# Optimization experiments

Measured on AMD Instinct MI355X. Metric: run time of the kernel, lower is better.

The kernel has to match this reference:

```python
import jax, jax.numpy as jnp
import numpy as np

HID, BOT, C, HEADS, K, SCALES, HZN = 32, 8, 16, 4, 3, 4, 12


def layer_norm(x, g, b, eps=1e-5):
    m = jnp.mean(x, axis=-1, keepdims=True)
    v = jnp.var(x, axis=-1, keepdims=True)
    return (x - m) * jax.lax.rsqrt(v + eps) * g + b


def setup_inputs() -> dict:
    B, T, N = 8, 32, 1500
    keys = iter(jax.random.split(jax.random.key(0), 64))
    def nrm(shape, s=0.05):
        return jax.random.normal(next(keys), shape, jnp.float32) * s
    x = jax.random.normal(next(keys), (B, T, N), jnp.float32)
    adj = (jax.random.uniform(next(keys), (N, N)) < 0.01).astype(jnp.float32)
    return dict(
        x=x, adj=adj,
        dw_w=nrm((1, 1, K)), dw_b=jnp.zeros((1,)),
        bn1_g=jnp.ones((1,)), bn1_b=jnp.zeros((1,)),
        pw_w=nrm((C, 1)), pw_b=jnp.zeros((C,)),
        bn2_g=jnp.ones((C,)), bn2_b=jnp.zeros((C,)),
        feat_w=nrm((C, HID)), feat_b=jnp.zeros((HID,)),
        scale_w=nrm((SCALES, HID, HID)), scale_b=jnp.zeros((SCALES, HID)),
        scale_ln_g=jnp.ones((SCALES, HID)), scale_ln_b=jnp.zeros((SCALES, HID)),
        fusion_weight=jnp.exp(-0.5 * jnp.arange(SCALES, dtype=jnp.float32)),
        fus_lo_w=nrm((HID, BOT)), fus_lo_b=jnp.zeros((BOT,)),
        fus_hi_w=nrm((BOT, HID)), fus_hi_b=jnp.zeros((HID,)),
        sp_ln_g=jnp.ones((HID,)), sp_ln_b=jnp.zeros((HID,)),
        qkv_lo_w=nrm((HID, 3 * BOT)), qkv_lo_b=jnp.zeros((3 * BOT,)),
        qkv_hi_w=nrm((3 * BOT, 3 * HID)), qkv_hi_b=jnp.zeros((3 * HID,)),
        graph_U=nrm((N, BOT)), graph_V=nrm((BOT, N)),
        adj_mix=jnp.array(0.0, jnp.float32), adj_scale=jnp.array(1.0, jnp.float32),
        out_lo_w=nrm((HID, BOT)), out_lo_b=jnp.zeros((BOT,)),
        out_hi_w=nrm((BOT, HID)), out_hi_b=jnp.zeros((HID,)),
        at_ln_g=jnp.ones((HID,)), at_ln_b=jnp.zeros((HID,)),
        pred_lo_w=nrm((HID, BOT)), pred_lo_b=jnp.zeros((BOT,)),
        mid_ln_g=jnp.ones((BOT,)), mid_ln_b=jnp.zeros((BOT,)),
        pred_hi_w=nrm((BOT, HZN)), pred_hi_b=jnp.zeros((HZN,)),
        log_decay=jnp.array(-2.3, jnp.float32),
        gate_w1=nrm((HID, BOT)), gate_b1=jnp.zeros((BOT,)),
        gate_w2=nrm((BOT, HZN)), gate_b2=jnp.zeros((HZN,)),
    )


def reference(x, adj, dw_w, dw_b, bn1_g, bn1_b, pw_w, pw_b, bn2_g, bn2_b,
              feat_w, feat_b, scale_w, scale_b, scale_ln_g, scale_ln_b,
              fusion_weight, fus_lo_w, fus_lo_b, fus_hi_w, fus_hi_b,
              sp_ln_g, sp_ln_b, qkv_lo_w, qkv_lo_b, qkv_hi_w, qkv_hi_b,
              graph_U, graph_V, adj_mix, adj_scale,
              out_lo_w, out_lo_b, out_hi_w, out_hi_b, at_ln_g, at_ln_b,
              pred_lo_w, pred_lo_b, mid_ln_g, mid_ln_b, pred_hi_w, pred_hi_b,
              log_decay, gate_w1, gate_b1, gate_w2, gate_b2):
    B, T, N = x.shape
    # ---- temporal feature extraction: depthwise-separable conv, eval-mode BN ----
    s = x.transpose(0, 2, 1).reshape(B * N, 1, T)  # per-node series [B*N,1,T]
    dw = jax.lax.conv_general_dilated(
        s, dw_w, (1,), 'SAME', dimension_numbers=('NCH', 'OIH', 'NCH'))
    dw = jax.nn.relu((dw + dw_b[None, :, None]) * bn1_g[None, :, None] + bn1_b[None, :, None])
    pw = jnp.einsum('bit,oi->bot', dw, pw_w) + pw_b[None, :, None]  # pointwise 1x1
    pw = jax.nn.relu(pw * bn2_g[None, :, None] + bn2_b[None, :, None])
    h = pw.mean(-1).reshape(B, N, C) @ feat_w + feat_b  # [B,N,HID]
    # ---- multi-scale spatial diffusion over adjacency powers ----
    eye = jnp.eye(N, dtype=x.dtype)
    a_hat = adj + eye
    a_hat = a_hat / (jnp.sum(a_hat, axis=-1, keepdims=True) + 1e-8)
    a2 = a_hat @ a_hat
    hops = [eye, a_hat, a2, a2 @ a_hat]
    feats = []
    for i in range(SCALES):  # fixed, small loop over scales
        agg = h if i == 0 else jnp.einsum('nm,bmh->bnh', hops[i], h)
        t = agg @ scale_w[i] + scale_b[i]
        feats.append(jax.nn.relu(layer_norm(t, scale_ln_g[i], scale_ln_b[i])))
    alpha = jax.nn.softmax(fusion_weight)
    fused = sum(alpha[i] * feats[i] for i in range(SCALES))
    out = (fused @ fus_lo_w + fus_lo_b) @ fus_hi_w + fus_hi_b  # bottleneck fusion
    h = layer_norm(out + h, sp_ln_g, sp_ln_b)
    # ---- low-rank adaptive graph attention ----
    qkv = (h @ qkv_lo_w + qkv_lo_b) @ qkv_hi_w + qkv_hi_b  # [B,N,3*HID]
    q, k, v = jnp.split(qkv, 3, axis=-1)
    hd = HID // HEADS
    to_heads = lambda t: t.reshape(B, N, HEADS, hd).transpose(0, 2, 1, 3)
    q, k, v = to_heads(q), to_heads(k), to_heads(v)
    scores = jnp.einsum('bhnd,bhmd->bhnm', q, k) / jnp.sqrt(jnp.float32(hd))
    struct = graph_U @ graph_V + jax.nn.sigmoid(adj_mix) * adj_scale * adj  # [N,N]
    attn = jax.nn.softmax(scores + struct[None, None], axis=-1)
    o = jnp.einsum('bhnm,bhmd->bhnd', attn, v).transpose(0, 2, 1, 3).reshape(B, N, HID)
    o = (o @ out_lo_w + out_lo_b) @ out_hi_w + out_hi_b
    h = layer_norm(o + h, at_ln_g, at_ln_b)
    # ---- gated horizon predictor with learned exponential decay ----
    x_mid = jax.nn.relu(layer_norm(h @ pred_lo_w + pred_lo_b, mid_ln_g, mid_ln_b))
    init_pred = x_mid @ pred_hi_w + pred_hi_b  # [B,N,HZN]
    gate = jax.nn.sigmoid(jax.nn.relu(h @ gate_w1 + gate_b1) @ gate_w2 + gate_b2)
    tdec = jnp.arange(1, HZN + 1, dtype=x.dtype)  # [HZN]
    prog = x[:, -1, :, None] * jnp.exp(-jnp.exp(log_decay) * tdec)
    return gate * init_pred + (1.0 - gate) * prog
```

## Files before the change

kernel.cpp:

```cpp
#include <hip/hip_runtime.h>
#include <math.h>

#define NN 1500
#define BB 8
#define TT 32
#define HIDD 32
#define BOTT 8
#define CC 16
#define NHEADS 4
#define NSCALES 4
#define HZNN 12
#define BC (BB*HIDD)
#define CAP 128
#define MC 128
#define MSPLIT 2
#define RT 128
#define NTILES 12
#define PROWS (NTILES*RT)

__global__ void k_prep_temporal(const float* __restrict__ adj,
                                const float* __restrict__ gV,
                                int* __restrict__ sidx, float* __restrict__ sval,
                                float* __restrict__ sraw, int* __restrict__ scnt,
                                float* __restrict__ VgT,
                                const float* __restrict__ x,
    const float* __restrict__ dw_w, const float* __restrict__ dw_b,
    const float* __restrict__ bn1_g, const float* __restrict__ bn1_b,
    const float* __restrict__ pw_w, const float* __restrict__ pw_b,
    const float* __restrict__ bn2_g, const float* __restrict__ bn2_b,
    const float* __restrict__ feat_w, const float* __restrict__ feat_b,
    float* __restrict__ h0) {
  if (blockIdx.x < NN) {
    int n = blockIdx.x;
    int tid = threadIdx.x;
    const float* row = adj + (size_t)n * NN;
    __shared__ int cnt;
    __shared__ float red[4];
    __shared__ float s_inv;
    float ssum = 0.f;
    for (int m = tid; m < NN; m += 256) ssum += row[m];
    for (int off = 32; off > 0; off >>= 1) ssum += __shfl_down(ssum, off, 64);
    if ((tid & 63) == 0) red[tid >> 6] = ssum;
    if (tid == 0) cnt = 0;
    __syncthreads();
    if (tid == 0) {
      float tot = red[0] + red[1] + red[2] + red[3] + 1.0f;
      s_inv = 1.0f / (tot + 1e-8f);
    }
    __syncthreads();
    float inv = s_inv;
    for (int m = tid; m < NN; m += 256) {
      float a = row[m];
      if (a != 0.f || m == n) {
        int pos = atomicAdd(&cnt, 1);
        if (pos < CAP) {
          sidx[n * CAP + pos] = m;
          sval[n * CAP + pos] = (a + (m == n ? 1.f : 0.f)) * inv;
          sraw[n * CAP + pos] = a;
        }
      }
    }
    __syncthreads();
    if (tid == 0) scnt[n] = min(cnt, CAP);
    if (n == 0) {
      for (int m = tid; m < NN; m += 256) {
#pragma unroll
        for (int j = 0; j < 8; ++j) VgT[m * 8 + j] = gV[j * NN + m];
      }
    }
  } else {
    int tid = (blockIdx.x - NN) * 256 + threadIdx.x;
    if (tid >= BB * NN) return;
    int b = tid / NN, n = tid % NN;
    float s[TT];
#pragma unroll
    for (int t = 0; t < TT; ++t) s[t] = x[(size_t)b * TT * NN + (size_t)t * NN + n];
    float w0 = dw_w[0], w1 = dw_w[1], w2 = dw_w[2];
    float db = dw_b[0], g1v = bn1_g[0], b1v = bn1_b[0];
    float dwr[TT];
#pragma unroll
    for (int t = 0; t < TT; ++t) {
      float left  = (t > 0)      ? s[t - 1] : 0.f;
      float right = (t < TT - 1) ? s[t + 1] : 0.f;
      float v = left * w0 + s[t] * w1 + right * w2;
      v = (v + db) * g1v + b1v;
      dwr[t] = fmaxf(v, 0.f);
    }
    float mo[CC];
#pragma unroll
    for (int o = 0; o < CC; ++o) mo[o] = 0.f;
    for (int t = 0; t < TT; ++t) {
      float d = dwr[t];
#pragma unroll
      for (int o = 0; o < CC; ++o) {
        float v = (d * pw_w[o] + pw_b[o]) * bn2_g[o] + bn2_b[o];
        mo[o] += fmaxf(v, 0.f);
      }
    }
#pragma unroll
    for (int o = 0; o < CC; ++o) mo[o] *= (1.f / TT);
    float* dst = h0 + (size_t)n * BC + b * HIDD;
    for (int j = 0; j < HIDD; ++j) {
      float acc = feat_b[j];
#pragma unroll
      for (int o = 0; o < CC; ++o) acc += mo[o] * feat_w[o * HIDD + j];
      dst[j] = acc;
    }
  }
}

__global__ void k_spmm_sp(const int* __restrict__ sidx, const float* __restrict__ sval,
                          const int* __restrict__ scnt,
                          const float* __restrict__ X, float* __restrict__ Y) {
  int n = blockIdx.x;
  int tid = threadIdx.x;
  __shared__ int   li[CAP];
  __shared__ float lv[CAP];
  int cnt = scnt[n];
  if (tid < cnt) { li[tid] = sidx[n * CAP + tid]; lv[tid] = sval[n * CAP + tid]; }
  __syncthreads();
  float acc = 0.f;
  for (int e = 0; e < cnt; ++e) acc += lv[e] * X[(size_t)li[e] * BC + tid];
  Y[(size_t)n * BC + tid] = acc;
}

__global__ void k_fuse_qkv(
    const float* __restrict__ h0, const float* __restrict__ g1,
    const float* __restrict__ g2, const float* __restrict__ g3,
    const float* __restrict__ scale_w, const float* __restrict__ scale_b,
    const float* __restrict__ sln_g, const float* __restrict__ sln_b,
    const float* __restrict__ fusion_w,
    const float* __restrict__ fus_lo_w, const float* __restrict__ fus_lo_b,
    const float* __restrict__ fus_hi_w, const float* __restrict__ fus_hi_b,
    const float* __restrict__ sp_g, const float* __restrict__ sp_b,
    const float* __restrict__ qkv_lo_w, const float* __restrict__ qkv_lo_b,
    const float* __restrict__ qkv_hi_w, const float* __restrict__ qkv_hi_b,
    float* __restrict__ h_out,
    float* __restrict__ Qw, float* __restrict__ Kw, float* __restrict__ Vw) {
  int tid = threadIdx.x;
  int gr = tid >> 4, l = tid & 15;
  int row = blockIdx.x * 16 + gr;
  int b = row / NN, n = row % NN;
  size_t rofs = (size_t)n * BC + b * HIDD;
  int j0 = 2 * l;
  float fw0 = fusion_w[0], fw1 = fusion_w[1], fw2 = fusion_w[2], fw3 = fusion_w[3];
  float fm = fmaxf(fmaxf(fw0, fw1), fmaxf(fw2, fw3));
  float e0 = __expf(fw0 - fm), e1 = __expf(fw1 - fm), e2 = __expf(fw2 - fm), e3 = __expf(fw3 - fm);
  float einv = 1.f / (e0 + e1 + e2 + e3);
  float alpha[4] = {e0 * einv, e1 * einv, e2 * einv, e3 * einv};
  const float* srcp[4] = {h0, g1, g2, g3};
  float fused[2] = {0.f, 0.f};
#pragma unroll
  for (int i = 0; i < NSCALES; ++i) {
    const float* sp = srcp[i] + rofs;
    float src[32];
#pragma unroll
    for (int k4 = 0; k4 < 8; ++k4) {
      float4 f = *(const float4*)(sp + k4 * 4);
      src[k4 * 4] = f.x; src[k4 * 4 + 1] = f.y; src[k4 * 4 + 2] = f.z; src[k4 * 4 + 3] = f.w;
    }
    const float* W = scale_w + i * HIDD * HIDD;
    float t0 = scale_b[i * HIDD + j0], t1v = scale_b[i * HIDD + j0 + 1];
#pragma unroll
    for (int k = 0; k < 32; ++k) {
      float2 w = *(const float2*)(W + k * HIDD + j0);
      t0 += src[k] * w.x; t1v += src[k] * w.y;
    }
    float s1 = t0 + t1v;
    float s2 = t0 * t0 + t1v * t1v;
    s1 += __shfl_xor(s1, 1, 16); s1 += __shfl_xor(s1, 2, 16);
    s1 += __shfl_xor(s1, 4, 16); s1 += __shfl_xor(s1, 8, 16);
    s2 += __shfl_xor(s2, 1, 16); s2 += __shfl_xor(s2, 2, 16);
    s2 += __shfl_xor(s2, 4, 16); s2 += __shfl_xor(s2, 8, 16);
    float mean = s1 * (1.f / 32.f);
    float var = s2 * (1.f / 32.f) - mean * mean;
    float r = rsqrtf(var + 1e-5f);
    float a = alpha[i];
    float tn0 = (t0 - mean) * r * sln_g[i * HIDD + j0] + sln_b[i * HIDD + j0];
    float tn1 = (t1v - mean) * r * sln_g[i * HIDD + j0 + 1] + sln_b[i * HIDD + j0 + 1];
    fused[0] += a * fmaxf(tn0, 0.f);
    fused[1] += a * fmaxf(tn1, 0.f);
  }
  float lo[BOTT];
#pragma unroll
  for (int o = 0; o < BOTT; ++o) {
    float acc = fused[0] * fus_lo_w[j0 * BOTT + o] + fused[1] * fus_lo_w[(j0 + 1) * BOTT + o];
    acc += __shfl_xor(acc, 1, 16); acc += __shfl_xor(acc, 2, 16);
    acc += __shfl_xor(acc, 4, 16); acc += __shfl_xor(acc, 8, 16);
    lo[o] = acc + fus_lo_b[o];
  }
  float2 hv2 = *(const float2*)(h0 + rofs + j0);
  float pre[2] = {hv2.x, hv2.y};
#pragma unroll
  for (int jj = 0; jj < 2; ++jj) {
    float acc = fus_hi_b[j0 + jj] + pre[jj];
#pragma unroll
    for (int o = 0; o < BOTT; ++o) acc += lo[o] * fus_hi_w[o * HIDD + j0 + jj];
    pre[jj] = acc;
  }
  {
    float s1 = pre[0] + pre[1];
    float s2 = pre[0] * pre[0] + pre[1] * pre[1];
    s1 += __shfl_xor(s1, 1, 16); s1 += __shfl_xor(s1, 2, 16);
    s1 += __shfl_xor(s1, 4, 16); s1 += __shfl_xor(s1, 8, 16);
    s2 += __shfl_xor(s2, 1, 16); s2 += __shfl_xor(s2, 2, 16);
    s2 += __shfl_xor(s2, 4, 16); s2 += __shfl_xor(s2, 8, 16);
    float mean = s1 * (1.f / 32.f);
    float var = s2 * (1.f / 32.f) - mean * mean;
    float r = rsqrtf(var + 1e-5f);
#pragma unroll
    for (int jj = 0; jj < 2; ++jj)
      pre[jj] = (pre[jj] - mean) * r * sp_g[j0 + jj] + sp_b[j0 + jj];
  }
  *(float2*)(h_out + (size_t)row * HIDD + j0) = make_float2(pre[0], pre[1]);
  float t1[24];
#pragma unroll
  for (int o = 0; o < 24; ++o) {
    float acc = pre[0] * qkv_lo_w[j0 * 24 + o] + pre[1] * qkv_lo_w[(j0 + 1) * 24 + o];
    acc += __shfl_xor(acc, 1, 16); acc += __shfl_xor(acc, 2, 16);
    acc += __shfl_xor(acc, 4, 16); acc += __shfl_xor(acc, 8, 16);
    t1[o] = acc + qkv_lo_b[o];
  }
  int sub = l >> 3, d = l & 7;
#pragma unroll
  for (int part = 0; part < 3; ++part) {
    float* dst = (part == 0) ? Qw : (part == 1) ? Kw : Vw;
#pragma unroll
    for (int hh = 0; hh < 2; ++hh) {
      int hd = sub * 2 + hh;
      int p = part * 32 + hd * 8 + d;
      float acc = qkv_hi_b[p];
#pragma unroll
      for (int o = 0; o < 24; ++o) acc += t1[o] * qkv_hi_w[o * 96 + p];
      dst[(((size_t)b * NHEADS + hd) * NN + n) * 8 + d] = acc;
    }
  }
}

__global__ void __launch_bounds__(256, 2)
k_attn(const float* __restrict__ Qw, const float* __restrict__ Kw,
       const float* __restrict__ Vw,
       const float* __restrict__ gU, const float* __restrict__ VgT,
       const int* __restrict__ sidx, const float* __restrict__ sraw,
       const int* __restrict__ scnt,
       const float* __restrict__ adj_mix, const float* __restrict__ adj_scale,
       float* __restrict__ P) {
  int bh = blockIdx.x, tile = blockIdx.y, z = blockIdx.z;
  int tid = threadIdx.x;
  int g = tid >> 3, p = tid & 7;
  __shared__ float Ks[MC * 20];
  __shared__ float Vs[MC * 12];
  const float scl = 0.35355339059327373f;
  float qv[4][16], acc[4][8], sm[4];
  int nrow[4];
#pragma unroll
  for (int rr = 0; rr < 4; ++rr) {
    int n = tile * RT + g * 4 + rr;
    nrow[rr] = n;
    int nc = (n < NN) ? n : NN - 1;
    const float* qp = Qw + ((size_t)bh * NN + nc) * 8;
    float4 q0 = *(const float4*)qp;
    float4 q1 = *(const float4*)(qp + 4);
    const float* up = gU + nc * 8;
    float4 u0 = *(const float4*)up;
    float4 u1 = *(const float4*)(up + 4);
    qv[rr][0] = q0.x * scl; qv[rr][1] = q0.y * scl; qv[rr][2] = q0.z * scl; qv[rr][3] = q0.w * scl;
    qv[rr][4] = q1.x * scl; qv[rr][5] = q1.y * scl; qv[rr][6] = q1.z * scl; qv[rr][7] = q1.w * scl;
    qv[rr][8] = u0.x; qv[rr][9] = u0.y; qv[rr][10] = u0.z; qv[rr][11] = u0.w;
    qv[rr][12] = u1.x; qv[rr][13] = u1.y; qv[rr][14] = u1.z; qv[rr][15] = u1.w;
    sm[rr] = 0.f;
#pragma unroll
    for (int d = 0; d < 8; ++d) acc[rr][d] = 0.f;
  }
  if (z < MSPLIT) {
    const int mcount = NN / MSPLIT;
    const int mbase = z * mcount;
    const float* Kb = Kw + (size_t)bh * NN * 8;
    const float* Vb = Vw + (size_t)bh * NN * 8;
    for (int c0 = 0; c0 < mcount; c0 += MC) {
      int mlen = min(MC, mcount - c0);
      __syncthreads();
      {
        int mm = tid >> 1, hh = tid & 1;
        float4 kf = make_float4(0.f,0.f,0.f,0.f), gf = kf, vf = kf;
        if (mm < mlen) {
          int m = mbase + c0 + mm;
          kf = *(const float4*)(Kb + (size_t)m * 8 + hh * 4);
          gf = *(const float4*)(VgT + (size_t)m * 8 + hh * 4);
          vf = *(const float4*)(Vb + (size_t)m * 8 + hh * 4);
        }
        *(float4*)(Ks + mm * 20 + hh * 4) = kf;
        *(float4*)(Ks + mm * 20 + 8 + hh * 4) = gf;
        *(float4*)(Vs + mm * 12 + hh * 4) = vf;
      }
      __syncthreads();
#pragma unroll 2
      for (int i = 0; i < MC / 8; ++i) {
        int mm = p + i * 8;
        const float* kp = Ks + mm * 20;
        float4 k0 = *(const float4*)(kp);
        float4 k1 = *(const float4*)(kp + 4);
        float4 k2 = *(const float4*)(kp + 8);
        float4 k3 = *(const float4*)(kp + 12);
        const float* vp = Vs + mm * 12;
        float4 v0 = *(const float4*)(vp);
        float4 v1 = *(const float4*)(vp + 4);
#pragma unroll
        for (int rr = 0; rr < 4; ++rr) {
          float s = qv[rr][0]*k0.x + qv[rr][1]*k0.y + qv[rr][2]*k0.z + qv[rr][3]*k0.w
                  + qv[rr][4]*k1.x + qv[rr][5]*k1.y + qv[rr][6]*k1.z + qv[rr][7]*k1.w
                  + qv[rr][8]*k2.x + qv[rr][9]*k2.y + qv[rr][10]*k2.z + qv[rr][11]*k2.w
                  + qv[rr][12]*k3.x + qv[rr][13]*k3.y + qv[rr][14]*k3.z + qv[rr][15]*k3.w;
          float e = __expf(s);
          sm[rr] += e;
          acc[rr][0] += e * v0.x; acc[rr][1] += e * v0.y; acc[rr][2] += e * v0.z; acc[rr][3] += e * v0.w;
          acc[rr][4] += e * v1.x; acc[rr][5] += e * v1.y; acc[rr][6] += e * v1.z; acc[rr][7] += e * v1.w;
        }
      }
      if (mlen < MC) {
        int npad = (MC / 8) - ((mlen - p + 7) >> 3);
#pragma unroll
        for (int rr = 0; rr < 4; ++rr) sm[rr] -= (float)npad;
      }
    }
  } else {
    float smix = adj_scale[0] / (1.f + __expf(-adj_mix[0]));
    const float* Kb = Kw + (size_t)bh * NN * 8;
    const float* Vb = Vw + (size_t)bh * NN * 8;
#pragma unroll
    for (int rr = 0; rr < 4; ++rr) {
      int n = nrow[rr];
      if (n < NN) {
        int cnt = scnt[n];
        for (int e = p; e < cnt; e += 8) {
          int m = sidx[n * CAP + e];
          float a = sraw[n * CAP + e];
          if (a != 0.f) {
            const float* kp = Kb + (size_t)m * 8;
            float4 k0 = *(const float4*)(kp);
            float4 k1 = *(const float4*)(kp + 4);
            const float* gp = VgT + (size_t)m * 8;
            float4 k2 = *(const float4*)(gp);
            float4 k3 = *(const float4*)(gp + 4);
            float s = qv[rr][0]*k0.x + qv[rr][1]*k0.y + qv[rr][2]*k0.z + qv[rr][3]*k0.w
                    + qv[rr][4]*k1.x + qv[rr][5]*k1.y + qv[rr][6]*k1.z + qv[rr][7]*k1.w
                    + qv[rr][8]*k2.x + qv[rr][9]*k2.y + qv[rr][10]*k2.z + qv[rr][11]*k2.w
                    + qv[rr][12]*k3.x + qv[rr][13]*k3.y + qv[rr][14]*k3.z + qv[rr][15]*k3.w;
            float ep = __expf(s);
            float dlt = ep * (__expf(smix * a) - 1.f);
            sm[rr] += dlt;
            const float* vp = Vb + (size_t)m * 8;
            float4 v0 = *(const float4*)(vp);
            float4 v1 = *(const float4*)(vp + 4);
            acc[rr][0] += dlt * v0.x; acc[rr][1] += dlt * v0.y; acc[rr][2] += dlt * v0.z; acc[rr][3] += dlt * v0.w;
            acc[rr][4] += dlt * v1.x; acc[rr][5] += dlt * v1.y; acc[rr][6] += dlt * v1.z; acc[rr][7] += dlt * v1.w;
          }
        }
      }
    }
  }
#pragma unroll
  for (int rr = 0; rr < 4; ++rr) {
    float s = sm[rr];
    s += __shfl_xor(s, 1, 8); s += __shfl_xor(s, 2, 8); s += __shfl_xor(s, 4, 8);
#pragma unroll
    for (int d = 0; d < 8; ++d) {
      acc[rr][d] += __shfl_xor(acc[rr][d], 1, 8);
      acc[rr][d] += __shfl_xor(acc[rr][d], 2, 8);
      acc[rr][d] += __shfl_xor(acc[rr][d], 4, 8);
    }
    float val = acc[rr][0];
#pragma unroll
    for (int d = 1; d < 8; ++d) if (p == d) val = acc[rr][d];
    if (nrow[rr] < NN) {
      float* dst = P + ((size_t)(z * 32 + bh) * PROWS + nrow[rr]) * 12;
      dst[p] = val;
      if (p == 0) dst[8] = s;
    }
  }
}

__global__ void k_final(const float* __restrict__ P, const float* __restrict__ h_in,
    const float* __restrict__ x,
    const float* __restrict__ out_lo_w, const float* __restrict__ out_lo_b,
    const float* __restrict__ out_hi_w, const float* __restrict__ out_hi_b,
    const float* __restrict__ at_g, const float* __restrict__ at_b,
    const float* __restrict__ pred_lo_w, const float* __restrict__ pred_lo_b,
    const float* __restrict__ mid_g, const float* __restrict__ mid_b,
    const float* __restrict__ pred_hi_w, const float* __restrict__ pred_hi_b,
    const float* __restrict__ log_decay,
    const float* __restrict__ gate_w1, const float* __restrict__ gate_b1,
    const float* __restrict__ gate_w2, const float* __restrict__ gate_b2,
    float* __restrict__ out) {
  int tid = threadIdx.x;
  int gr = tid >> 3, l = tid & 7;
  int row = blockIdx.x * 32 + gr;
  int b = row / NN, n = row % NN;
  int j0 = 4 * l;
  int hd = l >> 1, d0 = (l & 1) * 4;
  int bh = b * NHEADS + hd;
  float av[4] = {0.f, 0.f, 0.f, 0.f};
  float smt = 0.f;
#pragma unroll
  for (int z = 0; z <= MSPLIT; ++z) {
    const float* q = P + ((size_t)(z * 32 + bh) * PROWS + n) * 12;
    float4 a4 = *(const float4*)(q + d0);
    av[0] += a4.x; av[1] += a4.y; av[2] += a4.z; av[3] += a4.w;
    smt += q[8];
  }
  float oinv = 1.f / smt;
  float ov4[4];
#pragma unroll
  for (int d = 0; d < 4; ++d) ov4[d] = av[d] * oinv;
  float lo[BOTT];
#pragma unroll
  for (int o = 0; o < BOTT; ++o) {
    float acc = 0.f;
#pragma unroll
    for (int jj = 0; jj < 4; ++jj) acc += ov4[jj] * out_lo_w[(j0 + jj) * BOTT + o];
    acc += __shfl_xor(acc, 1, 8); acc += __shfl_xor(acc, 2, 8); acc += __shfl_xor(acc, 4, 8);
    lo[o] = acc + out_lo_b[o];
  }
  float4 hin4 = *(const float4*)(h_in + (size_t)row * HIDD + j0);
  float pre[4] = {hin4.x, hin4.y, hin4.z, hin4.w};
#pragma unroll
  for (int jj = 0; jj < 4; ++jj) {
    float acc = out_hi_b[j0 + jj] + pre[jj];
#pragma unroll
    for (int o = 0; o < BOTT; ++o) acc += lo[o] * out_hi_w[o * HIDD + j0 + jj];
    pre[jj] = acc;
  }
  float h2[4];
  {
    float s1 = pre[0] + pre[1] + pre[2] + pre[3];
    float s2 = pre[0]*pre[0] + pre[1]*pre[1] + pre[2]*pre[2] + pre[3]*pre[3];
    s1 += __shfl_xor(s1, 1, 8); s1 += __shfl_xor(s1, 2, 8); s1 += __shfl_xor(s1, 4, 8);
    s2 += __shfl_xor(s2, 1, 8); s2 += __shfl_xor(s2, 2, 8); s2 += __shfl_xor(s2, 4, 8);
    float mean = s1 * (1.f / 32.f);
    float var = s2 * (1.f / 32.f) - mean * mean;
    float r = rsqrtf(var + 1e-5f);
#pragma unroll
    for (int jj = 0; jj < 4; ++jj)
      h2[jj] = (pre[jj] - mean) * r * at_g[j0 + jj] + at_b[j0 + jj];
  }
  float pl[BOTT];
#pragma unroll
  for (int o = 0; o < BOTT; ++o) {
    float acc = 0.f;
#pragma unroll
    for (int jj = 0; jj < 4; ++jj) acc += h2[jj] * pred_lo_w[(j0 + jj) * BOTT + o];
    acc += __shfl_xor(acc, 1, 8); acc += __shfl_xor(acc, 2, 8); acc += __shfl_xor(acc, 4, 8);
    pl[o] = acc + pred_lo_b[o];
  }
  float xm[BOTT];
  {
    float m = 0.f;
#pragma unroll
    for (int o = 0; o < BOTT; ++o) m += pl[o];
    m *= (1.f / BOTT);
    float var = 0.f;
#pragma unroll
    for (int o = 0; o < BOTT; ++o) { float d = pl[o] - m; var += d * d; }
    var *= (1.f / BOTT);
    float r = rsqrtf(var + 1e-5f);
#pragma unroll
    for (int o = 0; o < BOTT; ++o)
      xm[o] = fmaxf((pl[o] - m) * r * mid_g[o] + mid_b[o], 0.f);
  }
  float ga[BOTT];
#pragma unroll
  for (int o = 0; o < BOTT; ++o) {
    float acc = 0.f;
#pragma unroll
    for (int jj = 0; jj < 4; ++jj) acc += h2[jj] * gate_w1[(j0 + jj) * BOTT + o];
    acc += __shfl_xor(acc, 1, 8); acc += __shfl_xor(acc, 2, 8); acc += __shfl_xor(acc, 4, 8);
    ga[o] = fmaxf(acc + gate_b1[o], 0.f);
  }
  float xl = x[(size_t)b * TT * NN + (size_t)(TT - 1) * NN + n];
  float dec = __expf(log_decay[0]);
#pragma unroll
  for (int ii = 0; ii < 2; ++ii) {
    int i = l + ii * 8;
    if (i < HZNN) {
      float accp = pred_hi_b[i];
#pragma unroll
      for (int o = 0; o < BOTT; ++o) accp += xm[o] * pred_hi_w[o * HZNN + i];
      float accg = gate_b2[i];
#pragma unroll
      for (int o = 0; o < BOTT; ++o) accg += ga[o] * gate_w2[o * HZNN + i];
      float gt = 1.f / (1.f + __expf(-accg));
      float pr = xl * __expf(-dec * (float)(i + 1));
      out[(size_t)row * HZNN + i] = gt * accp + (1.f - gt) * pr;
    }
  }
}

extern "C" void kernel_launch(void* const* d_in, const int* in_sizes, int n_in,
                              void* d_out, int out_size, void* d_ws, size_t ws_size,
                              hipStream_t stream) {
  const float* x          = (const float*)d_in[0];
  const float* adj        = (const float*)d_in[1];
  const float* dw_w       = (const float*)d_in[2];
  const float* dw_b       = (const float*)d_in[3];
  const float* bn1_g      = (const float*)d_in[4];
  const float* bn1_b      = (const float*)d_in[5];
  const float* pw_w       = (const float*)d_in[6];
  const float* pw_b       = (const float*)d_in[7];
  const float* bn2_g      = (const float*)d_in[8];
  const float* bn2_b      = (const float*)d_in[9];
  const float* feat_w     = (const float*)d_in[10];
  const float* feat_b     = (const float*)d_in[11];
  const float* scale_w    = (const float*)d_in[12];
  const float* scale_b    = (const float*)d_in[13];
  const float* scale_ln_g = (const float*)d_in[14];
  const float* scale_ln_b = (const float*)d_in[15];
  const float* fusion_w   = (const float*)d_in[16];
  const float* fus_lo_w   = (const float*)d_in[17];
  const float* fus_lo_b   = (const float*)d_in[18];
  const float* fus_hi_w   = (const float*)d_in[19];
  const float* fus_hi_b   = (const float*)d_in[20];
  const float* sp_ln_g    = (const float*)d_in[21];
  const float* sp_ln_b    = (const float*)d_in[22];
  const float* qkv_lo_w   = (const float*)d_in[23];
  const float* qkv_lo_b   = (const float*)d_in[24];
  const float* qkv_hi_w   = (const float*)d_in[25];
  const float* qkv_hi_b   = (const float*)d_in[26];
  const float* graph_U    = (const float*)d_in[27];
  const float* graph_V    = (const float*)d_in[28];
  const float* adj_mix    = (const float*)d_in[29];
  const float* adj_scale  = (const float*)d_in[30];
  const float* out_lo_w   = (const float*)d_in[31];
  const float* out_lo_b   = (const float*)d_in[32];
  const float* out_hi_w   = (const float*)d_in[33];
  const float* out_hi_b   = (const float*)d_in[34];
  const float* at_ln_g    = (const float*)d_in[35];
  const float* at_ln_b    = (const float*)d_in[36];
  const float* pred_lo_w  = (const float*)d_in[37];
  const float* pred_lo_b  = (const float*)d_in[38];
  const float* mid_ln_g   = (const float*)d_in[39];
  const float* mid_ln_b   = (const float*)d_in[40];
  const float* pred_hi_w  = (const float*)d_in[41];
  const float* pred_hi_b  = (const float*)d_in[42];
  const float* log_decay  = (const float*)d_in[43];
  const float* gate_w1    = (const float*)d_in[44];
  const float* gate_b1    = (const float*)d_in[45];
  const float* gate_w2    = (const float*)d_in[46];
  const float* gate_b2    = (const float*)d_in[47];

  float* ws = (float*)d_ws;
  float* h0    = ws;
  float* g1    = h0 + (size_t)NN * BC;
  float* g2    = g1 + (size_t)NN * BC;
  float* g3    = g2 + (size_t)NN * BC;
  float* hfull = g3 + (size_t)NN * BC;
  float* Qw    = hfull + (size_t)BB * NN * HIDD;
  float* Kw    = Qw + (size_t)BB * NN * HIDD;
  float* Vw    = Kw + (size_t)BB * NN * HIDD;
  float* VgT   = Vw + (size_t)BB * NN * HIDD;
  float* sval  = VgT + (size_t)NN * 8;
  float* sraw  = sval + (size_t)NN * CAP;
  int*   sidx  = (int*)(sraw + (size_t)NN * CAP);
  int*   scnt  = sidx + (size_t)NN * CAP;
  float* P     = (float*)(scnt + NN + 3);
  P = (float*)(((uintptr_t)P + 15) & ~(uintptr_t)15);

  k_prep_temporal<<<NN + 47, 256, 0, stream>>>(
      adj, graph_V, sidx, sval, sraw, scnt, VgT,
      x, dw_w, dw_b, bn1_g, bn1_b, pw_w, pw_b, bn2_g, bn2_b, feat_w, feat_b, h0);
  k_spmm_sp<<<NN, 256, 0, stream>>>(sidx, sval, scnt, h0, g1);
  k_spmm_sp<<<NN, 256, 0, stream>>>(sidx, sval, scnt, g1, g2);
  k_spmm_sp<<<NN, 256, 0, stream>>>(sidx, sval, scnt, g2, g3);
  k_fuse_qkv<<<(BB * NN) / 16, 256, 0, stream>>>(
      h0, g1, g2, g3, scale_w, scale_b, scale_ln_g, scale_ln_b, fusion_w,
      fus_lo_w, fus_lo_b, fus_hi_w, fus_hi_b, sp_ln_g, sp_ln_b,
      qkv_lo_w, qkv_lo_b, qkv_hi_w, qkv_hi_b, hfull, Qw, Kw, Vw);
  k_attn<<<dim3(32, NTILES, MSPLIT + 1), 256, 0, stream>>>(
      Qw, Kw, Vw, graph_U, VgT, sidx, sraw, scnt, adj_mix, adj_scale, P);
  k_final<<<(BB * NN) / 32, 256, 0, stream>>>(
      P, hfull, x, out_lo_w, out_lo_b, out_hi_w, out_hi_b, at_ln_g, at_ln_b,
      pred_lo_w, pred_lo_b, mid_ln_g, mid_ln_b, pred_hi_w, pred_hi_b,
      log_decay, gate_w1, gate_b1, gate_w2, gate_b2, (float*)d_out);
}
```

Baseline: 292.7 us.

## Move dense attention to fp16 MFMA and split sparse adjacency correction kernel

The dense part of the graph attention (QK^T plus low-rank U·V structural bias, exp, and P·V) is rewritten to use 16x16x16 fp16 MFMA instructions. Q/K are packed as 16-wide half vectors (scaled q plus U, k plus V^T), and V is stored transposed with an extra ones row so the softmax denominator is produced by the same MFMA. The sparse adjacency correction moves to its own kernel, and the fuse kernel now also writes the fp16 operands, with padding initialised in the prep kernel. This removes the scalar FP32 inner loop of the dense N×N attention, at the cost of fp16 rounding of scores and exponentials and no max-subtraction, which risks overflow or precision loss.

```diff
diff --git a/kernel.cpp b/kernel.cpp
--- a/kernel.cpp
+++ b/kernel.cpp
@@ -13,16 +13,21 @@
 #define BC (BB*HIDD)
 #define CAP 128
 #define MC 128
-#define MSPLIT 2
-#define RT 128
-#define NTILES 12
-#define PROWS (NTILES*RT)
+#define PROWS 1536
+#define KS_STRIDE 24
+#define VS_STRIDE 136
+
+typedef _Float16 f16;
+typedef __attribute__((ext_vector_type(4))) _Float16 half4;
+typedef __attribute__((ext_vector_type(4))) float floatx4;
 
 __global__ void k_prep_temporal(const float* __restrict__ adj,
                                 const float* __restrict__ gV,
                                 int* __restrict__ sidx, float* __restrict__ sval,
                                 float* __restrict__ sraw, int* __restrict__ scnt,
                                 float* __restrict__ VgT,
+                                f16* __restrict__ Qh, f16* __restrict__ Kh,
+                                f16* __restrict__ VT,
                                 const float* __restrict__ x,
     const float* __restrict__ dw_w, const float* __restrict__ dw_b,
     const float* __restrict__ bn1_g, const float* __restrict__ bn1_b,
@@ -68,6 +73,22 @@
         for (int j = 0; j < 8; ++j) VgT[m * 8 + j] = gV[j * NN + m];
       }
     }
+    if (n == 2) {
+      for (int idx = tid; idx < 32 * 36 * 16; idx += 256) {
+        int bb = idx / (36 * 16), rem = idx % (36 * 16);
+        size_t off = ((size_t)bb * PROWS + NN + rem / 16) * 16 + (rem % 16);
+        Qh[off] = (f16)0.f;
+        Kh[off] = (f16)0.f;
+      }
+      for (int idx = tid; idx < 32 * PROWS; idx += 256) {
+        int bb = idx / PROWS, m = idx % PROWS;
+        VT[((size_t)bb * 16 + 8) * PROWS + m] = (f16)((m < NN) ? 1.f : 0.f);
+      }
+      for (int idx = tid; idx < 32 * 8 * 36; idx += 256) {
+        int bb = idx / (8 * 36), rem = idx % (8 * 36);
+        VT[((size_t)bb * 16 + rem / 36) * PROWS + NN + (rem % 36)] = (f16)0.f;
+      }
+    }
   } else {
     int tid = (blockIdx.x - NN) * 256 + threadIdx.x;
     if (tid >= BB * NN) return;
@@ -135,8 +156,10 @@
     const float* __restrict__ sp_g, const float* __restrict__ sp_b,
     const float* __restrict__ qkv_lo_w, const float* __restrict__ qkv_lo_b,
     const float* __restrict__ qkv_hi_w, const float* __restrict__ qkv_hi_b,
+    const float* __restrict__ gU, const float* __restrict__ VgT,
     float* __restrict__ h_out,
-    float* __restrict__ Qw, float* __restrict__ Kw, float* __restrict__ Vw) {
+    float* __restrict__ Qw, float* __restrict__ Kw, float* __restrict__ Vw,
+    f16* __restrict__ Qh, f16* __restrict__ Kh, f16* __restrict__ VT) {
   int tid = threadIdx.x;
   int gr = tid >> 4, l = tid & 15;
   int row = blockIdx.x * 16 + gr;
@@ -221,6 +244,7 @@
     acc += __shfl_xor(acc, 4, 16); acc += __shfl_xor(acc, 8, 16);
     t1[o] = acc + qkv_lo_b[o];
   }
+  const float scl = 0.35355339059327373f;
   int sub = l >> 3, d = l & 7;
 #pragma unroll
   for (int part = 0; part < 3; ++part) {
@@ -233,149 +257,131 @@
 #pragma unroll
       for (int o = 0; o < 24; ++o) acc += t1[o] * qkv_hi_w[o * 96 + p];
       dst[(((size_t)b * NHEADS + hd) * NN + n) * 8 + d] = acc;
-    }
-  }
-}
-
-__global__ void __launch_bounds__(256, 2)
-k_attn(const float* __restrict__ Qw, const float* __restrict__ Kw,
-       const float* __restrict__ Vw,
-       const float* __restrict__ gU, const float* __restrict__ VgT,
-       const int* __restrict__ sidx, const float* __restrict__ sraw,
-       const int* __restrict__ scnt,
-       const float* __restrict__ adj_mix, const float* __restrict__ adj_scale,
-       float* __restrict__ P) {
-  int bh = blockIdx.x, tile = blockIdx.y, z = blockIdx.z;
+      int bh = b * NHEADS + hd;
+      if (part == 0) {
+        Qh[((size_t)bh * PROWS + n) * 16 + d] = (f16)(acc * scl);
+        Qh[((size_t)bh * PROWS + n) * 16 + 8 + d] = (f16)gU[n * 8 + d];
+      } else if (part == 1) {
+        Kh[((size_t)bh * PROWS + n) * 16 + d] = (f16)acc;
+        Kh[((size_t)bh * PROWS + n) * 16 + 8 + d] = (f16)VgT[n * 8 + d];
+      } else {
+        VT[((size_t)bh * 16 + d) * PROWS + n] = (f16)acc;
+      }
+    }
+  }
+}
+
+__global__ void __launch_bounds__(256, 4)
+k_attn_mfma(const f16* __restrict__ Qh, const f16* __restrict__ Kh,
+            const f16* __restrict__ VT, float* __restrict__ P) {
+  int bh = blockIdx.x;
+  int tile = blockIdx.y;
+  int tid = threadIdx.x;
+  int wave = tid >> 6, lane = tid & 63;
+  int quad = lane >> 4, l16 = lane & 15;
+  __shared__ f16 Ks[MC * KS_STRIDE];
+  __shared__ f16 Vs[16 * VS_STRIDE];
+  int n0 = tile * 64 + wave * 16;
+  half4 qf = *(const half4*)(Qh + ((size_t)bh * PROWS + n0 + l16) * 16 + quad * 4);
+  floatx4 acc = {0.f, 0.f, 0.f, 0.f};
+  for (int m0 = 0; m0 < PROWS; m0 += MC) {
+    __syncthreads();
+    {
+      int row = tid >> 1, h = (tid & 1) * 8;
+      *(float4*)(Ks + row * KS_STRIDE + h) =
+          *(const float4*)(Kh + ((size_t)bh * PROWS + m0 + row) * 16 + h);
+      int d = tid >> 4, c = (tid & 15) * 8;
+      *(float4*)(Vs + d * VS_STRIDE + c) =
+          *(const float4*)(VT + ((size_t)bh * 16 + d) * PROWS + m0 + c);
+    }
+    __syncthreads();
+#pragma unroll
+    for (int mt = 0; mt < MC / 16; ++mt) {
+      half4 kf = *(const half4*)(Ks + (mt * 16 + l16) * KS_STRIDE + quad * 4);
+      floatx4 s = __builtin_amdgcn_mfma_f32_16x16x16f16(
+          kf, qf, (floatx4){0.f, 0.f, 0.f, 0.f}, 0, 0, 0);
+      half4 pf;
+      pf[0] = (f16)__expf(s[0]);
+      pf[1] = (f16)__expf(s[1]);
+      pf[2] = (f16)__expf(s[2]);
+      pf[3] = (f16)__expf(s[3]);
+      half4 vf = *(const half4*)(Vs + l16 * VS_STRIDE + mt * 16 + quad * 4);
+      acc = __builtin_amdgcn_mfma_f32_16x16x16f16(pf, vf, acc, 0, 0, 0);
+    }
+  }
+  if (l16 < 9) {
+#pragma unroll
+    for (int r = 0; r < 4; ++r) {
+      int n = n0 + quad * 4 + r;
+      P[((size_t)bh * PROWS + n) * 12 + l16] = acc[r];
+    }
+  }
+}
+
+__global__ void k_attn_sp(const float* __restrict__ Qw, const float* __restrict__ Kw,
+                          const float* __restrict__ Vw,
+                          const float* __restrict__ gU, const float* __restrict__ VgT,
+                          const int* __restrict__ sidx, const float* __restrict__ sraw,
+                          const int* __restrict__ scnt,
+                          const float* __restrict__ adj_mix, const float* __restrict__ adj_scale,
+                          float* __restrict__ P) {
+  int bh = blockIdx.x;
   int tid = threadIdx.x;
   int g = tid >> 3, p = tid & 7;
-  __shared__ float Ks[MC * 20];
-  __shared__ float Vs[MC * 12];
+  float smix = adj_scale[0] / (1.f + __expf(-adj_mix[0]));
   const float scl = 0.35355339059327373f;
-  float qv[4][16], acc[4][8], sm[4];
-  int nrow[4];
-#pragma unroll
+  const float* Kb = Kw + (size_t)bh * NN * 8;
+  const float* Vb = Vw + (size_t)bh * NN * 8;
   for (int rr = 0; rr < 4; ++rr) {
-    int n = tile * RT + g * 4 + rr;
-    nrow[rr] = n;
-    int nc = (n < NN) ? n : NN - 1;
-    const float* qp = Qw + ((size_t)bh * NN + nc) * 8;
-    float4 q0 = *(const float4*)qp;
-    float4 q1 = *(const float4*)(qp + 4);
-    const float* up = gU + nc * 8;
-    float4 u0 = *(const float4*)up;
-    float4 u1 = *(const float4*)(up + 4);
-    qv[rr][0] = q0.x * scl; qv[rr][1] = q0.y * scl; qv[rr][2] = q0.z * scl; qv[rr][3] = q0.w * scl;
-    qv[rr][4] = q1.x * scl; qv[rr][5] = q1.y * scl; qv[rr][6] = q1.z * scl; qv[rr][7] = q1.w * scl;
-    qv[rr][8] = u0.x; qv[rr][9] = u0.y; qv[rr][10] = u0.z; qv[rr][11] = u0.w;
-    qv[rr][12] = u1.x; qv[rr][13] = u1.y; qv[rr][14] = u1.z; qv[rr][15] = u1.w;
-    sm[rr] = 0.f;
-#pragma unroll
-    for (int d = 0; d < 8; ++d) acc[rr][d] = 0.f;
-  }
-  if (z < MSPLIT) {
-    const int mcount = NN / MSPLIT;
-    const int mbase = z * mcount;
-    const float* Kb = Kw + (size_t)bh * NN * 8;
-    const float* Vb = Vw + (size_t)bh * NN * 8;
-    for (int c0 = 0; c0 < mcount; c0 += MC) {
-      int mlen = min(MC, mcount - c0);
-      __syncthreads();
-      {
-        int mm = tid >> 1, hh = tid & 1;
-        float4 kf = make_float4(0.f,0.f,0.f,0.f), gf = kf, vf = kf;
-        if (mm < mlen) {
-          int m = mbase + c0 + mm;
-          kf = *(const float4*)(Kb + (size_t)m * 8 + hh * 4);
-          gf = *(const float4*)(VgT + (size_t)m * 8 + hh * 4);
-          vf = *(const float4*)(Vb + (size_t)m * 8 + hh * 4);
+    int n = blockIdx.y * 128 + g * 4 + rr;
+    float acc[8] = {0.f, 0.f, 0.f, 0.f, 0.f, 0.f, 0.f, 0.f};
+    float sm = 0.f;
+    if (n < NN) {
+      const float* qp = Qw + ((size_t)bh * NN + n) * 8;
+      const float* up = gU + n * 8;
+      float qv[16];
+#pragma unroll
+      for (int d = 0; d < 8; ++d) { qv[d] = qp[d] * scl; qv[8 + d] = up[d]; }
+      int cnt = scnt[n];
+      for (int e = p; e < cnt; e += 8) {
+        int m = sidx[n * CAP + e];
+        float a = sraw[n * CAP + e];
+        if (a != 0.f) {
+          const float* kp = Kb + (size_t)m * 8;
+          float4 k0 = *(const float4*)(kp);
+          float4 k1 = *(const float4*)(kp + 4);
+          const float* gp = VgT + (size_t)m * 8;
+          float4 k2 = *(const float4*)(gp);
+          float4 k3 = *(const float4*)(gp + 4);
+          float s = qv[0]*k0.x + qv[1]*k0.y + qv[2]*k0.z + qv[3]*k0.w
+                  + qv[4]*k1.x + qv[5]*k1.y + qv[6]*k1.z + qv[7]*k1.w
+                  + qv[8]*k2.x + qv[9]*k2.y + qv[10]*k2.z + qv[11]*k2.w
+                  + qv[12]*k3.x + qv[13]*k3.y + qv[14]*k3.z + qv[15]*k3.w;
+          float ep = __expf(s);
+          float dlt = ep * (__expf(smix * a) - 1.f);
+          sm += dlt;
+          const float* vp = Vb + (size_t)m * 8;
+          float4 v0 = *(const float4*)(vp);
+          float4 v1 = *(const float4*)(vp + 4);
+          acc[0] += dlt * v0.x; acc[1] += dlt * v0.y; acc[2] += dlt * v0.z; acc[3] += dlt * v0.w;
+          acc[4] += dlt * v1.x; acc[5] += dlt * v1.y; acc[6] += dlt * v1.z; acc[7] += dlt * v1.w;
         }
-        *(float4*)(Ks + mm * 20 + hh * 4) = kf;
-        *(float4*)(Ks + mm * 20 + 8 + hh * 4) = gf;
-        *(float4*)(Vs + mm * 12 + hh * 4) = vf;
-      }
-      __syncthreads();
-#pragma unroll 2
-      for (int i = 0; i < MC / 8; ++i) {
-        int mm = p + i * 8;
-        const float* kp = Ks + mm * 20;
-        float4 k0 = *(const float4*)(kp);
-        float4 k1 = *(const float4*)(kp + 4);
-        float4 k2 = *(const float4*)(kp + 8);
-        float4 k3 = *(const float4*)(kp + 12);
-        const float* vp = Vs + mm * 12;
-        float4 v0 = *(const float4*)(vp);
-        float4 v1 = *(const float4*)(vp + 4);
-#pragma unroll
-        for (int rr = 0; rr < 4; ++rr) {
-          float s = qv[rr][0]*k0.x + qv[rr][1]*k0.y + qv[rr][2]*k0.z + qv[rr][3]*k0.w
-                  + qv[rr][4]*k1.x + qv[rr][5]*k1.y + qv[rr][6]*k1.z + qv[rr][7]*k1.w
-                  + qv[rr][8]*k2.x + qv[rr][9]*k2.y + qv[rr][10]*k2.z + qv[rr][11]*k2.w
-                  + qv[rr][12]*k3.x + qv[rr][13]*k3.y + qv[rr][14]*k3.z + qv[rr][15]*k3.w;
-          float e = __expf(s);
-          sm[rr] += e;
-          acc[rr][0] += e * v0.x; acc[rr][1] += e * v0.y; acc[rr][2] += e * v0.z; acc[rr][3] += e * v0.w;
-          acc[rr][4] += e * v1.x; acc[rr][5] += e * v1.y; acc[rr][6] += e * v1.z; acc[rr][7] += e * v1.w;
-        }
-      }
-      if (mlen < MC) {
-        int npad = (MC / 8) - ((mlen - p + 7) >> 3);
-#pragma unroll
-        for (int rr = 0; rr < 4; ++rr) sm[rr] -= (float)npad;
-      }
-    }
-  } else {
-    float smix = adj_scale[0] / (1.f + __expf(-adj_mix[0]));
-    const float* Kb = Kw + (size_t)bh * NN * 8;
-    const float* Vb = Vw + (size_t)bh * NN * 8;
-#pragma unroll
-    for (int rr = 0; rr < 4; ++rr) {
-      int n = nrow[rr];
-      if (n < NN) {
-        int cnt = scnt[n];
-        for (int e = p; e < cnt; e += 8) {
-          int m = sidx[n * CAP + e];
-          float a = sraw[n * CAP + e];
-          if (a != 0.f) {
-            const float* kp = Kb + (size_t)m * 8;
-            float4 k0 = *(const float4*)(kp);
-            float4 k1 = *(const float4*)(kp + 4);
-            const float* gp = VgT + (size_t)m * 8;
-            float4 k2 = *(const float4*)(gp);
-            float4 k3 = *(const float4*)(gp + 4);
-            float s = qv[rr][0]*k0.x + qv[rr][1]*k0.y + qv[rr][2]*k0.z + qv[rr][3]*k0.w
-                    + qv[rr][4]*k1.x + qv[rr][5]*k1.y + qv[rr][6]*k1.z + qv[rr][7]*k1.w
-                    + qv[rr][8]*k2.x + qv[rr][9]*k2.y + qv[rr][10]*k2.z + qv[rr][11]*k2.w
-                    + qv[rr][12]*k3.x + qv[rr][13]*k3.y + qv[rr][14]*k3.z + qv[rr][15]*k3.w;
-            float ep = __expf(s);
-            float dlt = ep * (__expf(smix * a) - 1.f);
-            sm[rr] += dlt;
-            const float* vp = Vb + (size_t)m * 8;
-            float4 v0 = *(const float4*)(vp);
-            float4 v1 = *(const float4*)(vp + 4);
-            acc[rr][0] += dlt * v0.x; acc[rr][1] += dlt * v0.y; acc[rr][2] += dlt * v0.z; acc[rr][3] += dlt * v0.w;
-            acc[rr][4] += dlt * v1.x; acc[rr][5] += dlt * v1.y; acc[rr][6] += dlt * v1.z; acc[rr][7] += dlt * v1.w;
-          }
-        }
-      }
-    }
-  }
-#pragma unroll
-  for (int rr = 0; rr < 4; ++rr) {
-    float s = sm[rr];
-    s += __shfl_xor(s, 1, 8); s += __shfl_xor(s, 2, 8); s += __shfl_xor(s, 4, 8);
+      }
+    }
+    sm += __shfl_xor(sm, 1, 8); sm += __shfl_xor(sm, 2, 8); sm += __shfl_xor(sm, 4, 8);
 #pragma unroll
     for (int d = 0; d < 8; ++d) {
-      acc[rr][d] += __shfl_xor(acc[rr][d], 1, 8);
-      acc[rr][d] += __shfl_xor(acc[rr][d], 2, 8);
-      acc[rr][d] += __shfl_xor(acc[rr][d], 4, 8);
-    }
-    float val = acc[rr][0];
-#pragma unroll
-    for (int d = 1; d < 8; ++d) if (p == d) val = acc[rr][d];
-    if (nrow[rr] < NN) {
-      float* dst = P + ((size_t)(z * 32 + bh) * PROWS + nrow[rr]) * 12;
+      acc[d] += __shfl_xor(acc[d], 1, 8);
+      acc[d] += __shfl_xor(acc[d], 2, 8);
+      acc[d] += __shfl_xor(acc[d], 4, 8);
+    }
+    float val = acc[0];
+#pragma unroll
+    for (int d = 1; d < 8; ++d) if (p == d) val = acc[d];
+    if (n < NN) {
+      float* dst = P + ((size_t)(32 + bh) * PROWS + n) * 12;
       dst[p] = val;
-      if (p == 0) dst[8] = s;
+      if (p == 0) dst[8] = sm;
     }
   }
 }
@@ -402,7 +408,7 @@
   float av[4] = {0.f, 0.f, 0.f, 0.f};
   float smt = 0.f;
 #pragma unroll
-  for (int z = 0; z <= MSPLIT; ++z) {
+  for (int z = 0; z < 2; ++z) {
     const float* q = P + ((size_t)(z * 32 + bh) * PROWS + n) * 12;
     float4 a4 = *(const float4*)(q + d0);
     av[0] += a4.x; av[1] += a4.y; av[2] += a4.z; av[3] += a4.w;
@@ -563,9 +569,12 @@
   int*   scnt  = sidx + (size_t)NN * CAP;
   float* P     = (float*)(scnt + NN + 3);
   P = (float*)(((uintptr_t)P + 15) & ~(uintptr_t)15);
+  f16* Qh = (f16*)(P + (size_t)2 * 32 * PROWS * 12);
+  f16* Kh = Qh + (size_t)32 * PROWS * 16;
+  f16* VT = Kh + (size_t)32 * PROWS * 16;
 
   k_prep_temporal<<<NN + 47, 256, 0, stream>>>(
-      adj, graph_V, sidx, sval, sraw, scnt, VgT,
+      adj, graph_V, sidx, sval, sraw, scnt, VgT, Qh, Kh, VT,
       x, dw_w, dw_b, bn1_g, bn1_b, pw_w, pw_b, bn2_g, bn2_b, feat_w, feat_b, h0);
   k_spmm_sp<<<NN, 256, 0, stream>>>(sidx, sval, scnt, h0, g1);
   k_spmm_sp<<<NN, 256, 0, stream>>>(sidx, sval, scnt, g1, g2);
@@ -573,8 +582,10 @@
   k_fuse_qkv<<<(BB * NN) / 16, 256, 0, stream>>>(
       h0, g1, g2, g3, scale_w, scale_b, scale_ln_g, scale_ln_b, fusion_w,
       fus_lo_w, fus_lo_b, fus_hi_w, fus_hi_b, sp_ln_g, sp_ln_b,
-      qkv_lo_w, qkv_lo_b, qkv_hi_w, qkv_hi_b, hfull, Qw, Kw, Vw);
-  k_attn<<<dim3(32, NTILES, MSPLIT + 1), 256, 0, stream>>>(
+      qkv_lo_w, qkv_lo_b, qkv_hi_w, qkv_hi_b, graph_U, VgT,
+      hfull, Qw, Kw, Vw, Qh, Kh, VT);
+  k_attn_mfma<<<dim3(32, PROWS / 64), 256, 0, stream>>>(Qh, Kh, VT, P);
+  k_attn_sp<<<dim3(32, 12), 256, 0, stream>>>(
       Qw, Kw, Vw, graph_U, VgT, sidx, sraw, scnt, adj_mix, adj_scale, P);
   k_final<<<(BB * NN) / 32, 256, 0, stream>>>(
       P, hfull, x, out_lo_w, out_lo_b, out_hi_w, out_hi_b, at_ln_g, at_ln_b,
```

New measurement: 255.6 us. 1.15x faster.
